# Optimization experiments

Measured on AMD Instinct MI355X. Metric: run time of the kernel, lower is better.

## Reference

```python
import jax
import jax.numpy as jnp
import numpy as np

B, C, H, W = 32, 192, 28, 28
OUT, K, GROUPS = 384, 9, 4


def setup_inputs() -> dict:
    key = jax.random.key(0)
    k1, k2, k3 = jax.random.split(key, 3)
    x = jax.random.normal(k1, (B, C, H, W), dtype=jnp.float32)
    # 1x1 grouped conv (groups=4): weight [out_channels, in_channels*2 // groups]
    weight = jax.random.normal(k2, (OUT, 2 * C // GROUPS), dtype=jnp.float32) * 0.05
    bias = jax.random.normal(k3, (OUT,), dtype=jnp.float32) * 0.05
    return {"x": x, "weight": weight, "bias": bias}


def _knn_indices(xf, k):
    """xf: [B, C, N] node features. Returns nn_idx [B, N, k] (no grad)."""
    xf = jax.lax.stop_gradient(xf)
    # L2-normalize along channel dim (F.normalize p=2 dim=1, eps=1e-12)
    nrm = jnp.sqrt(jnp.sum(xf * xf, axis=1, keepdims=True))
    xn = xf / jnp.maximum(nrm, 1e-12)
    pts = jnp.transpose(xn, (0, 2, 1))  # [B, N, C]
    sq = jnp.sum(pts * pts, axis=-1)  # [B, N]
    # dist = ||x_i||^2 - 2 x_i.y_j + ||y_j||^2
    dist = sq[:, :, None] - 2.0 * jnp.einsum("bnc,bmc->bnm", pts, pts) + sq[:, None, :]
    _, nn_idx = jax.lax.top_k(-dist, k)  # smallest distances -> [B, N, k]
    return nn_idx


def reference(x, weight, bias):
    b, c, h, w = x.shape
    n = h * w
    xf = x.reshape(b, c, n)  # [B, C, N]

    nn_idx = _knn_indices(xf, K)  # [B, N, K]

    feat = jnp.transpose(xf, (0, 2, 1))  # [B, N, C]
    # gather neighbor features: x_j [B, C, N, K]
    x_j = jax.vmap(lambda f, i: f[i])(feat, nn_idx)  # [B, N, K, C]
    x_j = jnp.transpose(x_j, (0, 3, 1, 2))  # [B, C, N, K]
    x_i = xf[:, :, :, None]  # [B, C, N, 1] (center = identity gather)

    # EdgeConv features: cat([x_i, x_j - x_i]) -> [B, 2C, N, K]
    edge = jnp.concatenate(
        [jnp.broadcast_to(x_i, x_j.shape), x_j - x_i], axis=1
    )

    # 1x1 grouped conv (groups=4) + bias + exact GELU
    cin_g = 2 * c // GROUPS
    cout_g = OUT // GROUPS
    eg = edge.reshape(b, GROUPS, cin_g, n, K)
    wg = weight.reshape(GROUPS, cout_g, cin_g)
    y = jnp.einsum("bgcnk,goc->bgonk", eg, wg).reshape(b, OUT, n, K)
    y = y + bias[None, :, None, None]
    y = jax.nn.gelu(y, approximate=False)

    # max over neighbors
    y = jnp.max(y, axis=-1)  # [B, OUT, N]
    return y.reshape(b, OUT, h, w)
```

## Files before the change

kernel.cpp:

```cpp
#include <hip/hip_runtime.h>
#include <math.h>

#define BSZ 32
#define CCH 192
#define NPIX 784
#define NP 896
#define NGRP 56
#define NGU 49
#define OUTC 384
#define KNN 9

typedef short s8v __attribute__((ext_vector_type(8)));
typedef float f4v __attribute__((ext_vector_type(4)));

#define XFH_BYTES ((size_t)BSZ * NGRP * 6 * 64 * 8 * 2)
#define XFL_BYTES XFH_BYTES
#define PAIR_BYTES ((size_t)BSZ * NP * 8)
#define IDX_BYTES ((size_t)BSZ * NPIX * KNN * 4)
#define TBUF_BYTES ((size_t)BSZ * 192 * NPIX * 4)
#define WF_BYTES ((size_t)24 * 3 * 64 * 8 * 2)

__device__ __forceinline__ float gelu_exact(float u) {
    return 0.5f * u * (1.0f + erff(u * 0.70710678118654752440f));
}
__device__ __forceinline__ ushort bf16_rne(float f) {
    uint u = __float_as_uint(f);
    uint r = (u + 0x7fffu + ((u >> 16) & 1u)) >> 16;
    return (ushort)r;
}
__device__ __forceinline__ float bf16f(ushort h) { return __uint_as_float(((uint)h) << 16); }

__global__ __launch_bounds__(64) void k0_wfrag(const float* __restrict__ w,
                                               ushort* __restrict__ wfh,
                                               ushort* __restrict__ wfl) {
    int c2 = blockIdx.x;
    int l = threadIdx.x;
    int ob = c2 / 3, kc = c2 - ob * 3;
    int row = ob * 16 + (l & 15);
    int k0c = kc * 32 + (l >> 4) * 8;
    const float* wr = w + row * 96 + k0c;
    s8v hv, lv;
#pragma unroll
    for (int k = 0; k < 8; ++k) {
        float v = wr[k];
        ushort h = bf16_rne(v);
        hv[k] = (short)h;
        lv[k] = (short)bf16_rne(v - bf16f(h));
    }
    *(s8v*)(wfh + ((size_t)c2 * 64 + l) * 8) = hv;
    *(s8v*)(wfl + ((size_t)c2 * 64 + l) * 8) = lv;
}

__global__ __launch_bounds__(256) void k1_normalize(const float* __restrict__ x,
                                                    ushort* __restrict__ xfh,
                                                    ushort* __restrict__ xfl,
                                                    float2* __restrict__ pair) {
    __shared__ float xs[CCH][65];
    int b = blockIdx.y;
    int n0 = blockIdx.x * 64;
    int t = threadIdx.x;
    const float* xb = x + (size_t)b * CCH * NPIX;

    for (int i = t; i < CCH * 64; i += 256) {
        int c = i >> 6, j = i & 63, n = n0 + j;
        xs[c][j] = (n < NPIX) ? xb[c * NPIX + n] : 0.f;
    }
    __syncthreads();

    {
        int j = t >> 2, part = t & 3;
        float ss = 0.f;
        for (int k = 0; k < 48; ++k) { float v = xs[part * 48 + k][j]; ss = fmaf(v, v, ss); }
        ss += __shfl_xor(ss, 1);
        ss += __shfl_xor(ss, 2);
        float inv = 1.0f / fmaxf(sqrtf(ss), 1e-12f);
        float s2 = 0.f;
        for (int k = 0; k < 48; ++k) {
            float v = xs[part * 48 + k][j] * inv;
            s2 = fmaf(v, v, s2);
        }
        s2 += __shfl_xor(s2, 1);
        s2 += __shfl_xor(s2, 2);
        if (part == 0) {
            int n = n0 + j;
            pair[b * NP + n] = (n < NPIX) ? make_float2(s2, inv) : make_float2(1e30f, 0.f);
        }
    }

#pragma unroll
    for (int i = 0; i < 6; ++i) {
        int ch = t + i * 256;
        int g = ch / 384, rem = ch - g * 384;
        int kc = rem >> 6, l = rem & 63;
        int nl = g * 16 + (l & 15);
        int c0 = kc * 32 + (l >> 4) * 8;
        s8v hv, lv;
#pragma unroll
        for (int k = 0; k < 8; ++k) {
            float v = xs[c0 + k][nl];
            ushort h = bf16_rne(v);
            hv[k] = (short)h;
            lv[k] = (short)bf16_rne(v - bf16f(h));
        }
        size_t doff = (((size_t)(b * NGRP + (n0 >> 4) + g)) * 6 + kc) * 512 + (size_t)l * 8;
        *(s8v*)(xfh + doff) = hv;
        *(s8v*)(xfl + doff) = lv;
    }
}

__device__ __forceinline__ bool lt_pair(float v, int id, float dv, int di) {
    return (v < dv) || (v == dv && id < di);
}
__device__ __forceinline__ void ins9p(float (&d)[KNN], int (&ii)[KNN], float v, int id) {
    if (!lt_pair(v, id, d[KNN - 1], ii[KNN - 1])) return;
    bool cprev = true;
#pragma unroll
    for (int p = KNN - 1; p >= 0; --p) {
        bool cp = (p == 0) ? false : lt_pair(v, id, d[p - 1], ii[p - 1]);
        float nd = cp ? d[p - 1] : (cprev ? v : d[p]);
        int nid = cp ? ii[p - 1] : (cprev ? id : ii[p]);
        d[p] = nd; ii[p] = nid; cprev = cp;
    }
}

__global__ __launch_bounds__(128, 3) void k2_knn(const ushort* __restrict__ xfh,
                                                 const ushort* __restrict__ xfl,
                                                 const float* __restrict__ pair,
                                                 int* __restrict__ nnidx) {
    __shared__ float dls[2][64][KNN];
    __shared__ int   ils[2][64][KNN];
    int wg = blockIdx.x;
    int b  = (wg & 7) * 4 + (wg >> 3) / 49;
    int qt = (wg >> 3) % 49;
    int t = threadIdx.x, w = t >> 6, l = t & 63;
    int lk = l >> 4;
    const ushort* fh = xfh + (size_t)b * NGRP * 3072;
    const ushort* fl = xfl + (size_t)b * NGRP * 3072;
    const float2* pb = (const float2*)(pair + (size_t)b * NP * 2);
    int l8 = l * 8;

    s8v qh[6], ql[6];
#pragma unroll
    for (int kc = 0; kc < 6; ++kc) {
        qh[kc] = *(const s8v*)(fh + (size_t)qt * 3072 + kc * 512 + l8);
        ql[kc] = *(const s8v*)(fl + (size_t)qt * 3072 + kc * 512 + l8);
    }
    float c2q = -2.f * pb[qt * 16 + (l & 15)].y;

    float d9[KNN]; int i9[KNN];
#pragma unroll
    for (int r = 0; r < KNN; ++r) { d9[r] = 3.4e38f; i9[r] = 0x7fffffff; }

    int g0 = w ? 24 : 0, g1 = w ? NGU : 24;
    for (int cg = g0; cg < g1; ++cg) {
        const ushort* ch = fh + (size_t)cg * 3072 + l8;
        const ushort* cl = fl + (size_t)cg * 3072 + l8;
        f4v aH  = {0.f, 0.f, 0.f, 0.f};
        f4v aX1 = {0.f, 0.f, 0.f, 0.f};
        f4v aX2 = {0.f, 0.f, 0.f, 0.f};
        f4v aX3 = {0.f, 0.f, 0.f, 0.f};
#pragma unroll
        for (int kc = 0; kc < 6; ++kc) {
            s8v vh = *(const s8v*)(ch + kc * 512);
            s8v vl = *(const s8v*)(cl + kc * 512);
            aH  = __builtin_amdgcn_mfma_f32_16x16x32_bf16(vh, qh[kc], aH,  0, 0, 0);
            aX1 = __builtin_amdgcn_mfma_f32_16x16x32_bf16(vl, qh[kc], aX1, 0, 0, 0);
            aX2 = __builtin_amdgcn_mfma_f32_16x16x32_bf16(vh, ql[kc], aX2, 0, 0, 0);
            aX3 = __builtin_amdgcn_mfma_f32_16x16x32_bf16(vl, ql[kc], aX3, 0, 0, 0);
        }
        float4 pA = *(const float4*)(pb + (size_t)(cg * 16 + lk * 4));
        float4 pB = *(const float4*)(pb + (size_t)(cg * 16 + lk * 4) + 2);
        float sqn_[4] = {pA.x, pA.z, pB.x, pB.z};
        float inv_[4] = {pA.y, pA.w, pB.y, pB.w};
#pragma unroll
        for (int r = 0; r < 4; ++r) {
            float v = fmaf(c2q * inv_[r], aH[r] + aX1[r] + aX2[r] + aX3[r], sqn_[r]);
            ins9p(d9, i9, v, cg * 16 + lk * 4 + r);
        }
    }

#pragma unroll
    for (int r = 0; r < KNN; ++r) { dls[w][l][r] = d9[r]; ils[w][l][r] = i9[r]; }
    __syncthreads();
    if (t < 16) {
        int q = qt * 16 + t;
        int pk[8] = {0, 0, 0, 0, 0, 0, 0, 0};
        int* op = nnidx + ((size_t)b * NPIX + q) * KNN;
        for (int r = 0; r < KNN; ++r) {
            float best = 3.4e38f; int bi = 0x7fffffff; int bk = 0;
#pragma unroll
            for (int m = 0; m < 8; ++m) {
                int ww = m >> 2, kk = m & 3;
                int idx = pk[m] < KNN ? pk[m] : KNN - 1;
                float v = dls[ww][kk * 16 + t][idx];
                int ii = ils[ww][kk * 16 + t][idx];
                if (pk[m] < KNN && lt_pair(v, ii, best, bi)) { best = v; bi = ii; bk = m; }
            }
            op[r] = bi;
#pragma unroll
            for (int m = 0; m < 8; ++m) pk[m] += (m == bk) ? 1 : 0;
        }
    }
}

__global__ __launch_bounds__(256, 2) void k3_proj(const ushort* __restrict__ xfh,
                                                  const ushort* __restrict__ xfl,
                                                  const ushort* __restrict__ wfh,
                                                  const ushort* __restrict__ wfl,
                                                  const float* __restrict__ bias,
                                                  float* __restrict__ out,
                                                  float* __restrict__ tbuf) {
    int wg = blockIdx.x;
    int b  = (wg & 7) * 4 + (wg >> 3) / 49;
    int ng = (wg >> 3) % 49;
    int t = threadIdx.x, g = t >> 6, l = t & 63;
    int h = l >> 4, m16 = l & 15;
    int kb = (g & 1) * 3;
    int l8 = l * 8;

    const ushort* fh = xfh + (((size_t)(b * NGRP + ng)) * 6 + kb) * 512 + l8;
    const ushort* fl = xfl + (((size_t)(b * NGRP + ng)) * 6 + kb) * 512 + l8;
    s8v xh[3], xl[3];
#pragma unroll
    for (int kk = 0; kk < 3; ++kk) {
        xh[kk] = *(const s8v*)(fh + kk * 512);
        xl[kk] = *(const s8v*)(fl + kk * 512);
    }

    for (int ogg = 0; ogg < 6; ++ogg) {
        int ob = g * 6 + ogg;
        const ushort* ph = wfh + ((size_t)ob * 3) * 512 + l8;
        const ushort* pl = wfl + ((size_t)ob * 3) * 512 + l8;
        f4v acc = {0.f, 0.f, 0.f, 0.f};
#pragma unroll
        for (int kk = 0; kk < 3; ++kk) {
            s8v wh = *(const s8v*)(ph + kk * 512);
            s8v wl = *(const s8v*)(pl + kk * 512);
            acc = __builtin_amdgcn_mfma_f32_16x16x32_bf16(xh[kk], wh, acc, 0, 0, 0);
            acc = __builtin_amdgcn_mfma_f32_16x16x32_bf16(xh[kk], wl, acc, 0, 0, 0);
            acc = __builtin_amdgcn_mfma_f32_16x16x32_bf16(xl[kk], wh, acc, 0, 0, 0);
        }
        int row = g * 96 + ogg * 16 + m16;
        if (g < 2) {
            float bv = bias[row];
#pragma unroll
            for (int r = 0; r < 4; ++r) {
                int n = ng * 16 + h * 4 + r;
                out[((size_t)b * OUTC + row) * NPIX + n] = gelu_exact(acc[r] + bv);
            }
        } else {
            int r2 = (g - 2) * 96 + ogg * 16 + m16;
#pragma unroll
            for (int r = 0; r < 4; ++r) {
                int n = ng * 16 + h * 4 + r;
                tbuf[((size_t)b * 192 + r2) * NPIX + n] = acc[r];
            }
        }
    }
}

__global__ __launch_bounds__(256) void k4_gather(const float* __restrict__ tbuf,
                                                 const int* __restrict__ nnidx,
                                                 const float* __restrict__ bias,
                                                 float* __restrict__ out) {
    __shared__ float trow[NPIX];
    int og2 = blockIdx.x;
    int b = blockIdx.y;
    int t = threadIdx.x;
    const float* tr = tbuf + ((size_t)b * 192 + og2) * NPIX;
    for (int i = t; i < NPIX; i += 256) trow[i] = tr[i];
    __syncthreads();
    float bv = bias[192 + og2];
    for (int n = t; n < NPIX; n += 256) {
        float ti = trow[n];
        const int* ip = nnidx + ((size_t)b * NPIX + n) * KNN;
        float umin = 3.4e38f, umax = -3.4e38f;
#pragma unroll
        for (int k = 0; k < KNN; ++k) {
            int j = ip[k];
            float u = trow[j] - ti + bv;
            umin = fminf(umin, u);
            umax = fmaxf(umax, u);
        }
        float m = fmaxf(gelu_exact(umin), gelu_exact(umax));
        out[((size_t)b * OUTC + 192 + og2) * NPIX + n] = m;
    }
}

extern "C" void kernel_launch(void* const* d_in, const int* in_sizes, int n_in,
                              void* d_out, int out_size, void* d_ws, size_t ws_size,
                              hipStream_t stream) {
    const float* x    = (const float*)d_in[0];
    const float* w    = (const float*)d_in[1];
    const float* bias = (const float*)d_in[2];
    float* out = (float*)d_out;
    char* ws = (char*)d_ws;

    ushort* xfh   = (ushort*)(ws);
    ushort* xfl   = (ushort*)(ws + XFH_BYTES);
    float2* pair  = (float2*)(ws + XFH_BYTES + XFL_BYTES);
    int*    nnidx = (int*)   (ws + XFH_BYTES + XFL_BYTES + PAIR_BYTES);
    float*  tbuf  = (float*) (ws + XFH_BYTES + XFL_BYTES + PAIR_BYTES + IDX_BYTES);
    ushort* wfh   = (ushort*)(ws + XFH_BYTES + XFL_BYTES + PAIR_BYTES + IDX_BYTES + TBUF_BYTES);
    ushort* wfl   = (ushort*)(ws + XFH_BYTES + XFL_BYTES + PAIR_BYTES + IDX_BYTES + TBUF_BYTES + WF_BYTES);

    k0_wfrag<<<dim3(72), 64, 0, stream>>>(w, wfh, wfl);
    k1_normalize<<<dim3(13, BSZ), 256, 0, stream>>>(x, xfh, xfl, pair);
    k2_knn<<<dim3(1568), 128, 0, stream>>>(xfh, xfl, (const float*)pair, nnidx);
    k3_proj<<<dim3(1568), 256, 0, stream>>>(xfh, xfl, wfh, wfl, bias, out, tbuf);
    k4_gather<<<dim3(192, BSZ), 256, 0, stream>>>(tbuf, nnidx, bias, out);
}
```

Before: 147.9 us.

## Use fast erf GELU, branchless top-9 insert, LDS-staged gather indices

Replaces exact erff GELU with an Abramowitz-Stegun polynomial using a hardware reciprocal and fast exp. It also rewrites the kNN top-9 insertion as a branchless parallel compare, dropping the early-exit and the index tie-break. The kNN loop is unrolled by two and its occupancy hint removed. The gather kernel stages the batch's neighbor indices in LDS with vector loads and remaps blocks to a 1D swizzled grid. The polynomial GELU has ~1e-7 absolute error, and losing the tie-break can change neighbor choice on equal distances.

Result: faster. 137.6 us (-6.9%).

```diff
diff --git a/kernel.cpp b/kernel.cpp
--- a/kernel.cpp
+++ b/kernel.cpp
@@ -20,15 +20,24 @@
 #define TBUF_BYTES ((size_t)BSZ * 192 * NPIX * 4)
 #define WF_BYTES ((size_t)24 * 3 * 64 * 8 * 2)
 
-__device__ __forceinline__ float gelu_exact(float u) {
-    return 0.5f * u * (1.0f + erff(u * 0.70710678118654752440f));
-}
 __device__ __forceinline__ ushort bf16_rne(float f) {
     uint u = __float_as_uint(f);
     uint r = (u + 0x7fffu + ((u >> 16) & 1u)) >> 16;
     return (ushort)r;
 }
 __device__ __forceinline__ float bf16f(ushort h) { return __uint_as_float(((uint)h) << 16); }
+
+__device__ __forceinline__ float gelu_fast(float u) {
+    float x = u * 0.70710678118654752440f;
+    float ax = fabsf(x);
+    float t = __builtin_amdgcn_rcpf(fmaf(0.3275911f, ax, 1.0f));
+    float p = t * fmaf(t, fmaf(t, fmaf(t, fmaf(t, 1.061405429f, -1.453152027f),
+                                       1.421413741f), -0.284496736f), 0.254829592f);
+    float e = __expf(-ax * ax);
+    float erf_ax = fmaf(-p, e, 1.0f);
+    float erfx = copysignf(erf_ax, x);
+    return 0.5f * u * (1.0f + erfx);
+}
 
 __global__ __launch_bounds__(64) void k0_wfrag(const float* __restrict__ w,
                                                ushort* __restrict__ wfh,
@@ -111,22 +120,26 @@
 __device__ __forceinline__ bool lt_pair(float v, int id, float dv, int di) {
     return (v < dv) || (v == dv && id < di);
 }
-__device__ __forceinline__ void ins9p(float (&d)[KNN], int (&ii)[KNN], float v, int id) {
-    if (!lt_pair(v, id, d[KNN - 1], ii[KNN - 1])) return;
-    bool cprev = true;
-#pragma unroll
-    for (int p = KNN - 1; p >= 0; --p) {
-        bool cp = (p == 0) ? false : lt_pair(v, id, d[p - 1], ii[p - 1]);
-        float nd = cp ? d[p - 1] : (cprev ? v : d[p]);
-        int nid = cp ? ii[p - 1] : (cprev ? id : ii[p]);
-        d[p] = nd; ii[p] = nid; cprev = cp;
-    }
-}
-
-__global__ __launch_bounds__(128, 3) void k2_knn(const ushort* __restrict__ xfh,
-                                                 const ushort* __restrict__ xfl,
-                                                 const float* __restrict__ pair,
-                                                 int* __restrict__ nnidx) {
+__device__ __forceinline__ void ins9b(float (&d)[KNN], int (&ii)[KNN], float v, int id) {
+    bool c[KNN];
+#pragma unroll
+    for (int p = 0; p < KNN; ++p) c[p] = v < d[p];
+    float nd[KNN]; int ni[KNN];
+    nd[0] = c[0] ? v : d[0];
+    ni[0] = c[0] ? id : ii[0];
+#pragma unroll
+    for (int p = 1; p < KNN; ++p) {
+        nd[p] = c[p - 1] ? d[p - 1] : (c[p] ? v : d[p]);
+        ni[p] = c[p - 1] ? ii[p - 1] : (c[p] ? id : ii[p]);
+    }
+#pragma unroll
+    for (int p = 0; p < KNN; ++p) { d[p] = nd[p]; ii[p] = ni[p]; }
+}
+
+__global__ __launch_bounds__(128) void k2_knn(const ushort* __restrict__ xfh,
+                                              const ushort* __restrict__ xfl,
+                                              const float* __restrict__ pair,
+                                              int* __restrict__ nnidx) {
     __shared__ float dls[2][64][KNN];
     __shared__ int   ils[2][64][KNN];
     int wg = blockIdx.x;
@@ -152,6 +165,7 @@
     for (int r = 0; r < KNN; ++r) { d9[r] = 3.4e38f; i9[r] = 0x7fffffff; }
 
     int g0 = w ? 24 : 0, g1 = w ? NGU : 24;
+#pragma unroll 2
     for (int cg = g0; cg < g1; ++cg) {
         const ushort* ch = fh + (size_t)cg * 3072 + l8;
         const ushort* cl = fl + (size_t)cg * 3072 + l8;
@@ -175,7 +189,7 @@
 #pragma unroll
         for (int r = 0; r < 4; ++r) {
             float v = fmaf(c2q * inv_[r], aH[r] + aX1[r] + aX2[r] + aX3[r], sqn_[r]);
-            ins9p(d9, i9, v, cg * 16 + lk * 4 + r);
+            ins9b(d9, i9, v, cg * 16 + lk * 4 + r);
         }
     }
 
@@ -246,7 +260,7 @@
 #pragma unroll
             for (int r = 0; r < 4; ++r) {
                 int n = ng * 16 + h * 4 + r;
-                out[((size_t)b * OUTC + row) * NPIX + n] = gelu_exact(acc[r] + bv);
+                out[((size_t)b * OUTC + row) * NPIX + n] = gelu_fast(acc[r] + bv);
             }
         } else {
             int r2 = (g - 2) * 96 + ogg * 16 + m16;
@@ -264,16 +278,21 @@
                                                  const float* __restrict__ bias,
                                                  float* __restrict__ out) {
     __shared__ float trow[NPIX];
-    int og2 = blockIdx.x;
-    int b = blockIdx.y;
+    __shared__ int nn[NPIX * KNN];
+    int wg = blockIdx.x;
+    int b   = (wg & 7) * 4 + (wg >> 3) / 192;
+    int og2 = (wg >> 3) % 192;
     int t = threadIdx.x;
-    const float* tr = tbuf + ((size_t)b * 192 + og2) * NPIX;
-    for (int i = t; i < NPIX; i += 256) trow[i] = tr[i];
+    const float4* tr4 = (const float4*)(tbuf + ((size_t)b * 192 + og2) * NPIX);
+    for (int i = t; i < NPIX / 4; i += 256) ((float4*)trow)[i] = tr4[i];
+    const int4* nb4 = (const int4*)(nnidx + (size_t)b * NPIX * KNN);
+    for (int i = t; i < NPIX * KNN / 4; i += 256) ((int4*)nn)[i] = nb4[i];
     __syncthreads();
     float bv = bias[192 + og2];
+    float* orow = out + ((size_t)b * OUTC + 192 + og2) * NPIX;
     for (int n = t; n < NPIX; n += 256) {
         float ti = trow[n];
-        const int* ip = nnidx + ((size_t)b * NPIX + n) * KNN;
+        const int* ip = nn + n * KNN;
         float umin = 3.4e38f, umax = -3.4e38f;
 #pragma unroll
         for (int k = 0; k < KNN; ++k) {
@@ -282,8 +301,7 @@
             umin = fminf(umin, u);
             umax = fmaxf(umax, u);
         }
-        float m = fmaxf(gelu_exact(umin), gelu_exact(umax));
-        out[((size_t)b * OUTC + 192 + og2) * NPIX + n] = m;
+        orow[n] = fmaxf(gelu_fast(umin), gelu_fast(umax));
     }
 }
 
@@ -308,5 +326,5 @@
     k1_normalize<<<dim3(13, BSZ), 256, 0, stream>>>(x, xfh, xfl, pair);
     k2_knn<<<dim3(1568), 128, 0, stream>>>(xfh, xfl, (const float*)pair, nnidx);
     k3_proj<<<dim3(1568), 256, 0, stream>>>(xfh, xfl, wfh, wfl, bias, out, tbuf);
-    k4_gather<<<dim3(192, BSZ), 256, 0, stream>>>(tbuf, nnidx, bias, out);
-}
+    k4_gather<<<dim3(6144), 256, 0, stream>>>(tbuf, nnidx, bias, out);
+}
```
